# Kernel optimization log

Hardware: AMD Instinct MI355X
Metric: run time of the kernel (lower is better)

The kernel has to match this reference:

```python
import math
import jax, jax.numpy as jnp
import numpy as np

B, T, D = 2, 2048, 1024
NH = 16
HD = D // NH


def setup_inputs() -> dict:
    key = jax.random.key(0)
    k1, k2, k3 = jax.random.split(key, 3)
    s = 0.02
    return {
        "x": jax.random.normal(k1, (B, T, D), dtype=jnp.float32),
        "w_qkv": jax.random.normal(k2, (D, 3 * D), dtype=jnp.float32) * s,
        "w_proj": jax.random.normal(k3, (D, D), dtype=jnp.float32) * s,
    }


def reference(x, w_qkv, w_proj):
    b, t, c = x.shape
    qkv = x @ w_qkv  # [B,T,3D]
    q, k, v = jnp.split(qkv, 3, axis=-1)
    # [B,NH,T,HD]
    q = q.reshape(b, t, NH, HD).transpose(0, 2, 1, 3)
    k = k.reshape(b, t, NH, HD).transpose(0, 2, 1, 3)
    v = v.reshape(b, t, NH, HD).transpose(0, 2, 1, 3)
    scores = jnp.einsum("bhqd,bhkd->bhqk", q, k) / math.sqrt(HD)
    mask = jnp.tril(jnp.ones((t, t), dtype=x.dtype))  # [T,T]
    # faithful to source: scaled scores are multiplied by the mask, then -1e9 added where masked
    masked = scores * mask + (1.0 - mask) * (-1e9)
    a = jax.nn.softmax(masked, axis=-1)
    out = jnp.einsum("bhqk,bhkd->bhqd", a, v)  # [B,NH,T,HD]
    out = out.transpose(0, 2, 1, 3).reshape(b, t, c)
    return out @ w_proj
```

## Files before the change

### kernel.cpp

```cpp
#include <hip/hip_runtime.h>
#include <stdint.h>

#define B_SZ 2
#define T_SEQ 2048
#define D_MODEL 1024
#define NHEADS 16
#define HDIM 64
#define QKV_P (3 * D_MODEL)

typedef unsigned short u16;
typedef uint32_t u32;
typedef __attribute__((ext_vector_type(4))) float f32x4;
typedef __attribute__((ext_vector_type(8))) short s16x8;
typedef __attribute__((ext_vector_type(4))) short s16x4;

__device__ __forceinline__ u16 f2bf(float f) {
  union { float f; uint32_t u; } v; v.f = f;
  uint32_t r = v.u + 0x7fffu + ((v.u >> 16) & 1u);
  return (u16)(r >> 16);
}

__device__ __forceinline__ float fastexp2(float x) {
  float r;
  asm volatile("v_exp_f32 %0, %1" : "=v"(r) : "v"(x));
  return r;
}

__device__ __forceinline__ u32 cvtpk(float lo, float hi) {
  u32 r;
  asm volatile("v_cvt_pk_bf16_f32 %0, %1, %2" : "=v"(r) : "v"(lo), "v"(hi));
  return r;
}

__device__ __forceinline__ void async16(const void* g, void* l) {
  __builtin_amdgcn_global_load_lds((const __attribute__((address_space(1))) void*)g,
                                   (__attribute__((address_space(3))) void*)l,
                                   16, 0, 0);
}

__global__ void convert_bf16_kernel(const float* __restrict__ in, u16* __restrict__ out, int n4) {
  int i = blockIdx.x * blockDim.x + threadIdx.x;
  if (i < n4) {
    float4 v = ((const float4*)in)[i];
    ushort4 o;
    o.x = f2bf(v.x); o.y = f2bf(v.y); o.z = f2bf(v.z); o.w = f2bf(v.w);
    ((ushort4*)out)[i] = o;
  }
}

__global__ void transpose_convert(const float* __restrict__ in, u16* __restrict__ out, int R, int C) {
  __shared__ float tile[32][33];
  const int tx = threadIdx.x, ty = threadIdx.y;
  const int c0 = blockIdx.x * 32, r0 = blockIdx.y * 32;
#pragma unroll
  for (int i = 0; i < 4; i++)
    tile[ty + i * 8][tx] = in[(size_t)(r0 + ty + i * 8) * C + c0 + tx];
  __syncthreads();
#pragma unroll
  for (int i = 0; i < 4; i++)
    out[(size_t)(c0 + ty + i * 8) * R + r0 + tx] = f2bf(tile[tx][ty + i * 8]);
}

__global__ void transpose_v(const u16* __restrict__ qkv, u16* __restrict__ vT) {
  __shared__ u16 tile[32][33];
  const int tx = threadIdx.x, ty = threadIdx.y;
  const int tt = blockIdx.x * 32;
  const int bh = blockIdx.y >> 1, hdt = blockIdx.y & 1;
  const int b = bh >> 4, h = bh & 15;
  const int hh = hdt * 32;
#pragma unroll
  for (int i = 0; i < 4; i++)
    tile[ty + i * 8][tx] =
        qkv[(size_t)(b * T_SEQ + tt + ty + i * 8) * QKV_P + 2 * D_MODEL + h * HDIM + hh + tx];
  __syncthreads();
#pragma unroll
  for (int i = 0; i < 4; i++)
    vT[(size_t)(bh * HDIM + hh + ty + i * 8) * T_SEQ + tt + tx] = tile[tx][ty + i * 8];
}

template <int F32OUT>
__global__ __launch_bounds__(256) void gemm_bt(const u16* __restrict__ A,
                                               const u16* __restrict__ BT,
                                               void* __restrict__ Cout,
                                               int M, int N, int K) {
  __shared__ u16 As[128 * 32];
  __shared__ u16 Bs[128 * 32];
  const int tid = threadIdx.x;
  const int lane = tid & 63, w = tid >> 6;
  const int l15 = lane & 15, g = lane >> 4;
  const int wr = w >> 1, wc = w & 1;
  const int bn = blockIdx.x, bm = blockIdx.y;
  const u16* Ab = A + (size_t)bm * 128 * K;
  const u16* Bb = BT + (size_t)bn * 128 * K;
  f32x4 acc[4][4];
#pragma unroll
  for (int i = 0; i < 4; i++)
#pragma unroll
    for (int j = 0; j < 4; j++) acc[i][j] = (f32x4){0.f, 0.f, 0.f, 0.f};
  const int c0 = tid, c1 = tid + 256;
  for (int kt = 0; kt < K; kt += 32) {
    async16(Ab + (size_t)(c0 >> 2) * K + kt + (c0 & 3) * 8, (char*)As + c0 * 16);
    async16(Ab + (size_t)(c1 >> 2) * K + kt + (c1 & 3) * 8, (char*)As + c1 * 16);
    async16(Bb + (size_t)(c0 >> 2) * K + kt + (c0 & 3) * 8, (char*)Bs + c0 * 16);
    async16(Bb + (size_t)(c1 >> 2) * K + kt + (c1 & 3) * 8, (char*)Bs + c1 * 16);
    asm volatile("s_waitcnt vmcnt(0)" ::: "memory");
    __syncthreads();
    s16x8 af[4], bfr[4];
#pragma unroll
    for (int i = 0; i < 4; i++)
      af[i] = *(const s16x8*)(As + (wr * 64 + i * 16 + l15) * 32 + g * 8);
#pragma unroll
    for (int j = 0; j < 4; j++)
      bfr[j] = *(const s16x8*)(Bs + (wc * 64 + j * 16 + l15) * 32 + g * 8);
#pragma unroll
    for (int i = 0; i < 4; i++)
#pragma unroll
      for (int j = 0; j < 4; j++)
        acc[i][j] = __builtin_amdgcn_mfma_f32_16x16x32_bf16(af[i], bfr[j], acc[i][j], 0, 0, 0);
    __syncthreads();
  }
#pragma unroll
  for (int i = 0; i < 4; i++) {
    const int row0 = bm * 128 + wr * 64 + i * 16 + g * 4;
#pragma unroll
    for (int j = 0; j < 4; j++) {
      const int col = bn * 128 + wc * 64 + j * 16 + l15;
#pragma unroll
      for (int r = 0; r < 4; r++) {
        if (F32OUT)
          ((float*)Cout)[(size_t)(row0 + r) * N + col] = acc[i][j][r];
        else
          ((u16*)Cout)[(size_t)(row0 + r) * N + col] = f2bf(acc[i][j][r]);
      }
    }
  }
}

__global__ __launch_bounds__(256, 3) void flash_attn(const u16* __restrict__ qkv,
                                                     const u16* __restrict__ vT,
                                                     u16* __restrict__ attn) {
  __shared__ u16 Ks[2][64 * 64];
  __shared__ u16 Vs[2][64 * 64];
  const int tid = threadIdx.x;
  const int lane = tid & 63, w = tid >> 6;
  const int l15 = lane & 15, g = lane >> 4;
  const int id = blockIdx.x;
  const int bh = ((id & 7) << 2) | ((id >> 3) & 3);
  const int qs = 31 - (id >> 5);
  const int b = bh >> 4, h = bh & 15;

  const size_t qrow = (size_t)(b * T_SEQ + qs * 64 + w * 16 + l15);
  s16x8 qf[2];
  qf[0] = *(const s16x8*)(qkv + qrow * QKV_P + h * HDIM + 0 * 32 + g * 8);
  qf[1] = *(const s16x8*)(qkv + qrow * QKV_P + h * HDIM + 1 * 32 + g * 8);

  f32x4 O[4];
#pragma unroll
  for (int t = 0; t < 4; t++) O[t] = (f32x4){0.f, 0.f, 0.f, 0.f};
  float m_s = -1e30f, l_s = 0.f;
  const int qrl = w * 16 + l15;
  const float sc = 0.18033688011112042f;

#define STAGE(buf, kvt_)                                                                     \
  do {                                                                                       \
    _Pragma("unroll") for (int i_ = 0; i_ < 2; i_++) {                                       \
      int o_ = (tid + i_ * 256) * 16;                                                        \
      int lo_ = o_ ^ (((o_ >> 7) & 7) << 4);                                                 \
      int row_ = lo_ >> 7;                                                                   \
      int byt_ = lo_ & 127;                                                                  \
      async16(qkv + (size_t)(b * T_SEQ + (kvt_) * 64 + row_) * QKV_P + D_MODEL + h * HDIM +  \
                  (byt_ >> 1),                                                               \
              (char*)Ks[buf] + o_);                                                          \
      async16(vT + (size_t)(bh * HDIM + row_) * T_SEQ + (kvt_) * 64 + (byt_ >> 1),           \
              (char*)Vs[buf] + o_);                                                          \
    }                                                                                        \
  } while (0)

  STAGE(0, 0);
  int cur = 0;
  const int nt = qs + 1;
  for (int kvt = 0; kvt < nt; ++kvt) {
    if (kvt < qs) {
      STAGE(cur ^ 1, kvt + 1);
      asm volatile("s_waitcnt vmcnt(4)" ::: "memory");
    } else {
      asm volatile("s_waitcnt vmcnt(0)" ::: "memory");
    }
    __syncthreads();

    f32x4 S[4];
#pragma unroll
    for (int t16 = 0; t16 < 4; t16++) S[t16] = (f32x4){0.f, 0.f, 0.f, 0.f};
#pragma unroll
    for (int t16 = 0; t16 < 4; t16++)
#pragma unroll
      for (int kk = 0; kk < 2; kk++) {
        int key = t16 * 16 + l15;
        int bp = (key * 128 + kk * 64 + g * 16) ^ ((key & 7) << 4);
        s16x8 kf = *(const s16x8*)((const char*)Ks[cur] + bp);
        S[t16] = __builtin_amdgcn_mfma_f32_16x16x32_bf16(kf, qf[kk], S[t16], 0, 0, 0);
      }

    if (kvt == qs) {
#pragma unroll
      for (int t16 = 0; t16 < 4; t16++)
#pragma unroll
        for (int r = 0; r < 4; r++)
          if (t16 * 16 + g * 4 + r > qrl) S[t16][r] = -3e38f;
    }
    float mx = fmaxf(fmaxf(fmaxf(S[0][0], S[0][1]), fmaxf(S[0][2], S[0][3])),
                     fmaxf(fmaxf(S[1][0], S[1][1]), fmaxf(S[1][2], S[1][3])));
    mx = fmaxf(mx, fmaxf(fmaxf(fmaxf(S[2][0], S[2][1]), fmaxf(S[2][2], S[2][3])),
                         fmaxf(fmaxf(S[3][0], S[3][1]), fmaxf(S[3][2], S[3][3]))));
    mx = fmaxf(mx, __shfl_xor(mx, 16));
    mx = fmaxf(mx, __shfl_xor(mx, 32));
    if (!__all(mx - m_s <= 40.f)) {
      const float mnew = fmaxf(m_s, mx);
      const float alpha = fastexp2((m_s - mnew) * sc);
      m_s = mnew;
      l_s *= alpha;
#pragma unroll
      for (int t = 0; t < 4; t++)
#pragma unroll
        for (int r = 0; r < 4; r++) O[t][r] *= alpha;
    }
    const float msc = m_s * sc;
    float p[16];
#pragma unroll
    for (int t16 = 0; t16 < 4; t16++)
#pragma unroll
      for (int r = 0; r < 4; r++) p[t16 * 4 + r] = fastexp2(fmaf(S[t16][r], sc, -msc));
    float ps = 0.f;
#pragma unroll
    for (int i = 0; i < 16; i++) ps += p[i];
    ps += __shfl_xor(ps, 16);
    ps += __shfl_xor(ps, 32);
    l_s += ps;

#pragma unroll
    for (int t16 = 0; t16 < 4; t16++) {
      union { u32 u[2]; s16x4 v; } pbv;
      pbv.u[0] = cvtpk(p[t16 * 4 + 0], p[t16 * 4 + 1]);
      pbv.u[1] = cvtpk(p[t16 * 4 + 2], p[t16 * 4 + 3]);
#pragma unroll
      for (int t = 0; t < 4; t++) {
        int hd = t * 16 + l15;
        int bp = (hd * 128 + t16 * 32 + g * 8) ^ ((hd & 7) << 4);
        s16x4 vf = *(const s16x4*)((const char*)Vs[cur] + bp);
        O[t] = __builtin_amdgcn_mfma_f32_16x16x16bf16_1k(vf, pbv.v, O[t], 0, 0, 0);
      }
    }
    __syncthreads();
    cur ^= 1;
  }

  const float inv = 1.0f / l_s;
  const size_t row = (size_t)(b * T_SEQ + qs * 64 + w * 16 + l15);
#pragma unroll
  for (int t = 0; t < 4; t++)
#pragma unroll
    for (int pr = 0; pr < 2; pr++) {
      u32 pk = cvtpk(O[t][pr * 2 + 0] * inv, O[t][pr * 2 + 1] * inv);
      *(u32*)&attn[row * D_MODEL + h * HDIM + t * 16 + g * 4 + pr * 2] = pk;
    }
}

extern "C" void kernel_launch(void* const* d_in, const int* in_sizes, int n_in,
                              void* d_out, int out_size, void* d_ws, size_t ws_size,
                              hipStream_t stream) {
  const float* x = (const float*)d_in[0];
  const float* w_qkv = (const float*)d_in[1];
  const float* w_proj = (const float*)d_in[2];
  float* out = (float*)d_out;
  char* ws = (char*)d_ws;
  const size_t MB = (size_t)1 << 20;
  if (ws_size < 56 * MB) return;
  u16* xb = (u16*)(ws + 0);
  u16* wqkvT = (u16*)(ws + 8 * MB);
  u16* wprojT = (u16*)(ws + 14 * MB);
  u16* qkv = (u16*)(ws + 16 * MB);
  u16* vT = (u16*)(ws + 40 * MB);
  u16* attn = (u16*)(ws + 48 * MB);

  convert_bf16_kernel<<<4096, 256, 0, stream>>>(x, xb, (B_SZ * T_SEQ * D_MODEL) / 4);
  transpose_convert<<<dim3(96, 32), dim3(32, 8), 0, stream>>>(w_qkv, wqkvT, D_MODEL, QKV_P);
  transpose_convert<<<dim3(32, 32), dim3(32, 8), 0, stream>>>(w_proj, wprojT, D_MODEL, D_MODEL);
  gemm_bt<0><<<dim3(QKV_P / 128, (B_SZ * T_SEQ) / 128), 256, 0, stream>>>(
      xb, wqkvT, qkv, B_SZ * T_SEQ, QKV_P, D_MODEL);
  transpose_v<<<dim3(T_SEQ / 32, B_SZ * NHEADS * 2), dim3(32, 8), 0, stream>>>(qkv, vT);
  flash_attn<<<1024, 256, 0, stream>>>(qkv, vT, attn);
  gemm_bt<1><<<dim3(D_MODEL / 128, (B_SZ * T_SEQ) / 128), 256, 0, stream>>>(
      attn, wprojT, out, B_SZ * T_SEQ, D_MODEL, D_MODEL);
}
```

Baseline: 127.9 us.

## Fuse prep kernels, double-buffer GEMM loads, write V transposed from QKV GEMM

Merges the x conversion and both weight transpose-converts into one prep kernel. The GEMM now double-buffers its LDS tiles so global loads for the next K step overlap the MFMA work on the current one. The QKV GEMM writes the V block straight into the transposed vT layout, which removes the separate transpose_v pass. Together these cut launch count and an extra read and write of V, at the cost of doubled LDS use per block and scattered 8-byte stores for vT.

```diff
diff --git a/kernel.cpp b/kernel.cpp
--- a/kernel.cpp
+++ b/kernel.cpp
@@ -38,53 +38,47 @@
                                    16, 0, 0);
 }
 
-__global__ void convert_bf16_kernel(const float* __restrict__ in, u16* __restrict__ out, int n4) {
-  int i = blockIdx.x * blockDim.x + threadIdx.x;
-  if (i < n4) {
-    float4 v = ((const float4*)in)[i];
+__global__ __launch_bounds__(256) void prep(const float* __restrict__ x,
+                                            const float* __restrict__ wq,
+                                            const float* __restrict__ wp,
+                                            u16* __restrict__ xb,
+                                            u16* __restrict__ wqkvT,
+                                            u16* __restrict__ wprojT) {
+  const int bid = blockIdx.x, tid = threadIdx.x;
+  if (bid < 4096) {
+    int i = bid * 256 + tid;
+    float4 v = ((const float4*)x)[i];
     ushort4 o;
     o.x = f2bf(v.x); o.y = f2bf(v.y); o.z = f2bf(v.z); o.w = f2bf(v.w);
-    ((ushort4*)out)[i] = o;
-  }
-}
-
-__global__ void transpose_convert(const float* __restrict__ in, u16* __restrict__ out, int R, int C) {
+    ((ushort4*)xb)[i] = o;
+    return;
+  }
   __shared__ float tile[32][33];
-  const int tx = threadIdx.x, ty = threadIdx.y;
-  const int c0 = blockIdx.x * 32, r0 = blockIdx.y * 32;
+  const float* in; u16* outp; int C, bx, by;
+  if (bid < 4096 + 3072) {
+    int bb = bid - 4096; in = wq; outp = wqkvT; C = 3072; bx = bb % 96; by = bb / 96;
+  } else {
+    int bb = bid - 7168; in = wp; outp = wprojT; C = 1024; bx = bb % 32; by = bb / 32;
+  }
+  const int tx = tid & 31, ty = tid >> 5;
+  const int c0 = bx * 32, r0 = by * 32;
 #pragma unroll
   for (int i = 0; i < 4; i++)
     tile[ty + i * 8][tx] = in[(size_t)(r0 + ty + i * 8) * C + c0 + tx];
   __syncthreads();
 #pragma unroll
   for (int i = 0; i < 4; i++)
-    out[(size_t)(c0 + ty + i * 8) * R + r0 + tx] = f2bf(tile[tx][ty + i * 8]);
-}
-
-__global__ void transpose_v(const u16* __restrict__ qkv, u16* __restrict__ vT) {
-  __shared__ u16 tile[32][33];
-  const int tx = threadIdx.x, ty = threadIdx.y;
-  const int tt = blockIdx.x * 32;
-  const int bh = blockIdx.y >> 1, hdt = blockIdx.y & 1;
-  const int b = bh >> 4, h = bh & 15;
-  const int hh = hdt * 32;
-#pragma unroll
-  for (int i = 0; i < 4; i++)
-    tile[ty + i * 8][tx] =
-        qkv[(size_t)(b * T_SEQ + tt + ty + i * 8) * QKV_P + 2 * D_MODEL + h * HDIM + hh + tx];
-  __syncthreads();
-#pragma unroll
-  for (int i = 0; i < 4; i++)
-    vT[(size_t)(bh * HDIM + hh + ty + i * 8) * T_SEQ + tt + tx] = tile[tx][ty + i * 8];
-}
-
-template <int F32OUT>
+    outp[(size_t)(c0 + ty + i * 8) * D_MODEL + r0 + tx] = f2bf(tile[tx][ty + i * 8]);
+}
+
+template <int F32OUT, int VFUSE>
 __global__ __launch_bounds__(256) void gemm_bt(const u16* __restrict__ A,
                                                const u16* __restrict__ BT,
                                                void* __restrict__ Cout,
+                                               u16* __restrict__ vTout,
                                                int M, int N, int K) {
-  __shared__ u16 As[128 * 32];
-  __shared__ u16 Bs[128 * 32];
+  __shared__ u16 As[2][128 * 32];
+  __shared__ u16 Bs[2][128 * 32];
   const int tid = threadIdx.x;
   const int lane = tid & 63, w = tid >> 6;
   const int l15 = lane & 15, g = lane >> 4;
@@ -98,26 +92,57 @@
 #pragma unroll
     for (int j = 0; j < 4; j++) acc[i][j] = (f32x4){0.f, 0.f, 0.f, 0.f};
   const int c0 = tid, c1 = tid + 256;
+
+#define GSTAGE(buf, kt_)                                                          \
+  do {                                                                            \
+    async16(Ab + (size_t)(c0 >> 2) * K + (kt_) + (c0 & 3) * 8, (char*)As[buf] + c0 * 16); \
+    async16(Ab + (size_t)(c1 >> 2) * K + (kt_) + (c1 & 3) * 8, (char*)As[buf] + c1 * 16); \
+    async16(Bb + (size_t)(c0 >> 2) * K + (kt_) + (c0 & 3) * 8, (char*)Bs[buf] + c0 * 16); \
+    async16(Bb + (size_t)(c1 >> 2) * K + (kt_) + (c1 & 3) * 8, (char*)Bs[buf] + c1 * 16); \
+  } while (0)
+
+  GSTAGE(0, 0);
+  int cur = 0;
   for (int kt = 0; kt < K; kt += 32) {
-    async16(Ab + (size_t)(c0 >> 2) * K + kt + (c0 & 3) * 8, (char*)As + c0 * 16);
-    async16(Ab + (size_t)(c1 >> 2) * K + kt + (c1 & 3) * 8, (char*)As + c1 * 16);
-    async16(Bb + (size_t)(c0 >> 2) * K + kt + (c0 & 3) * 8, (char*)Bs + c0 * 16);
-    async16(Bb + (size_t)(c1 >> 2) * K + kt + (c1 & 3) * 8, (char*)Bs + c1 * 16);
-    asm volatile("s_waitcnt vmcnt(0)" ::: "memory");
+    if (kt + 32 < K) {
+      GSTAGE(cur ^ 1, kt + 32);
+      asm volatile("s_waitcnt vmcnt(4)" ::: "memory");
+    } else {
+      asm volatile("s_waitcnt vmcnt(0)" ::: "memory");
+    }
     __syncthreads();
     s16x8 af[4], bfr[4];
 #pragma unroll
     for (int i = 0; i < 4; i++)
-      af[i] = *(const s16x8*)(As + (wr * 64 + i * 16 + l15) * 32 + g * 8);
+      af[i] = *(const s16x8*)(As[cur] + (wr * 64 + i * 16 + l15) * 32 + g * 8);
 #pragma unroll
     for (int j = 0; j < 4; j++)
-      bfr[j] = *(const s16x8*)(Bs + (wc * 64 + j * 16 + l15) * 32 + g * 8);
+      bfr[j] = *(const s16x8*)(Bs[cur] + (wc * 64 + j * 16 + l15) * 32 + g * 8);
 #pragma unroll
     for (int i = 0; i < 4; i++)
 #pragma unroll
       for (int j = 0; j < 4; j++)
         acc[i][j] = __builtin_amdgcn_mfma_f32_16x16x32_bf16(af[i], bfr[j], acc[i][j], 0, 0, 0);
     __syncthreads();
+    cur ^= 1;
+  }
+
+  if (VFUSE && bn >= 16) {
+    const int bloc = bm >> 4;
+    const int tb = bm * 128 + wr * 64 - bloc * T_SEQ;
+#pragma unroll
+    for (int i = 0; i < 4; i++) {
+      const int tl = tb + i * 16 + g * 4;
+#pragma unroll
+      for (int j = 0; j < 4; j++) {
+        const int hh = bn * 128 + wc * 64 + j * 16 + l15 - 2048;
+        uint2 pk;
+        pk.x = cvtpk(acc[i][j][0], acc[i][j][1]);
+        pk.y = cvtpk(acc[i][j][2], acc[i][j][3]);
+        *(uint2*)&vTout[(size_t)(bloc * 1024 + hh) * T_SEQ + tl] = pk;
+      }
+    }
+    return;
   }
 #pragma unroll
   for (int i = 0; i < 4; i++) {
@@ -282,13 +307,10 @@
   u16* vT = (u16*)(ws + 40 * MB);
   u16* attn = (u16*)(ws + 48 * MB);
 
-  convert_bf16_kernel<<<4096, 256, 0, stream>>>(x, xb, (B_SZ * T_SEQ * D_MODEL) / 4);
-  transpose_convert<<<dim3(96, 32), dim3(32, 8), 0, stream>>>(w_qkv, wqkvT, D_MODEL, QKV_P);
-  transpose_convert<<<dim3(32, 32), dim3(32, 8), 0, stream>>>(w_proj, wprojT, D_MODEL, D_MODEL);
-  gemm_bt<0><<<dim3(QKV_P / 128, (B_SZ * T_SEQ) / 128), 256, 0, stream>>>(
-      xb, wqkvT, qkv, B_SZ * T_SEQ, QKV_P, D_MODEL);
-  transpose_v<<<dim3(T_SEQ / 32, B_SZ * NHEADS * 2), dim3(32, 8), 0, stream>>>(qkv, vT);
+  prep<<<8192, 256, 0, stream>>>(x, w_qkv, w_proj, xb, wqkvT, wprojT);
+  gemm_bt<0, 1><<<dim3(QKV_P / 128, (B_SZ * T_SEQ) / 128), 256, 0, stream>>>(
+      xb, wqkvT, qkv, vT, B_SZ * T_SEQ, QKV_P, D_MODEL);
   flash_attn<<<1024, 256, 0, stream>>>(qkv, vT, attn);
-  gemm_bt<1><<<dim3(D_MODEL / 128, (B_SZ * T_SEQ) / 128), 256, 0, stream>>>(
-      attn, wprojT, out, B_SZ * T_SEQ, D_MODEL, D_MODEL);
-}
+  gemm_bt<1, 0><<<dim3(D_MODEL / 128, (B_SZ * T_SEQ) / 128), 256, 0, stream>>>(
+      attn, wprojT, out, nullptr, B_SZ * T_SEQ, D_MODEL, D_MODEL);
+}
```

Result: faster. 114.7 us (-10.3%).
